# Performance work log

Measured on AMD Instinct MI355X. Metric: run time of the kernel, lower is better.

## Reference

```python
import jax, jax.numpy as jnp
import numpy as np

ALPHA_U = 1.0 / 10.0   # dt/tauu
ALPHA_V = 1.0 / 150.0  # dt/tauv
M = 10.0

def setup_inputs() -> dict:
    key = jax.random.key(0)
    ks = jax.random.split(key, 6)
    B, D_in, H = 8192, 1024, 2048
    stdv = 1.0 / np.sqrt(H)
    return {
        "x": jax.random.normal(ks[0], (B, D_in), dtype=jnp.float32),
        "u": jax.random.normal(ks[1], (B, H), dtype=jnp.float32),
        "v": jax.random.normal(ks[2], (B, H), dtype=jnp.float32),
        "win": jax.random.uniform(ks[3], (H, D_in), dtype=jnp.float32, minval=-stdv, maxval=stdv),
        "wr": jax.random.uniform(ks[4], (H, H), dtype=jnp.float32, minval=-stdv, maxval=stdv),
        "bias": jax.random.uniform(ks[5], (H,), dtype=jnp.float32, minval=-stdv, maxval=stdv),
    }

def reference(x, u, v, win, wr, bias):
    # v update: leaky blend toward m*u, then relu
    v_new = jax.nn.relu((1.0 - ALPHA_V) * v + (ALPHA_V * M) * u)
    # u update: leaky blend with input + recurrent drive minus adapted v
    drive = jnp.einsum('bi,hi->bh', x, win) + jnp.einsum('bk,hk->bh', u, wr) + bias - v_new
    u_new = jax.nn.relu((1.0 - ALPHA_U) * u + ALPHA_U * drive)
    return (u_new, v_new)
```

## Files before the change

### kernel.cpp

```cpp
#include <hip/hip_runtime.h>
#include <hip/hip_bf16.h>
#include <stdint.h>

#define B_DIM 8192
#define D_IN  1024
#define H_DIM 2048
#define K_DIM (D_IN + H_DIM)

#define CV_CONST  (1.0f - 1.0f/150.0f)
#define CUV_CONST (10.0f/150.0f)
#define CU_CONST  0.9f
#define AU_CONST  0.1f

typedef __attribute__((ext_vector_type(8))) short short8;
typedef __attribute__((ext_vector_type(4))) float floatx4;

__device__ __forceinline__ unsigned short f2bf(float f) {
    union { float f; unsigned u; } x; x.f = f;
    unsigned r = x.u + 0x7fffu + ((x.u >> 16) & 1u);
    return (unsigned short)(r >> 16);
}

#define N4_X   ((B_DIM * D_IN)  / 4)
#define N4_U   ((B_DIM * H_DIM) / 4)
#define N4_WIN ((H_DIM * D_IN)  / 4)
#define N4_WR  ((H_DIM * H_DIM) / 4)
#define N4_TOT (N4_X + N4_U + N4_WIN + N4_WR)

__global__ __launch_bounds__(256)
void pack_all(const float4* __restrict__ x, const float4* __restrict__ u,
              const float4* __restrict__ win, const float4* __restrict__ wr,
              unsigned short* __restrict__ Abf, unsigned short* __restrict__ Wbf) {
    int i = blockIdx.x * 256 + threadIdx.x;
    const float4* src; unsigned short* dst; int shift, mask, coloff;
    if (i < N4_X)                    { src = x;   dst = Abf; shift = 10; mask = 1023; coloff = 0;    }
    else if (i < N4_X + N4_U)        { i -= N4_X; src = u;   dst = Abf; shift = 11; mask = 2047; coloff = D_IN; }
    else if (i < N4_X + N4_U + N4_WIN){ i -= N4_X + N4_U; src = win; dst = Wbf; shift = 10; mask = 1023; coloff = 0; }
    else                             { i -= N4_X + N4_U + N4_WIN; src = wr; dst = Wbf; shift = 11; mask = 2047; coloff = D_IN; }
    int idx = i << 2;
    int r = idx >> shift;
    int c = idx & mask;
    float4 f = src[i];
    ushort4 o;
    o.x = f2bf(f.x); o.y = f2bf(f.y); o.z = f2bf(f.z); o.w = f2bf(f.w);
    *(ushort4*)(dst + (size_t)r * K_DIM + coloff + c) = o;
}

#define GLOAD_LDS16(gp, lp)                                                          \
    __builtin_amdgcn_global_load_lds(                                                \
        (const __attribute__((address_space(1))) unsigned int*)(gp),                 \
        (__attribute__((address_space(3))) unsigned int*)(lp), 16, 0, 0)

#define ES_STRIDE 68
#define ES_REGION (16 * ES_STRIDE)
#define SMEM_BYTES (8 * ES_REGION * 4)

__global__ __launch_bounds__(256, 4)
void gemm_fused(const unsigned short* __restrict__ A,
                const unsigned short* __restrict__ Wc,
                const float* __restrict__ u_in,
                const float* __restrict__ v_in,
                const float* __restrict__ bias,
                float* __restrict__ out)
{
    __shared__ __align__(16) unsigned char smem_raw[SMEM_BYTES];
    unsigned short* As = (unsigned short*)smem_raw;
    unsigned short* Bs = As + 128 * 32;
    float* Esf = (float*)smem_raw;

    const int tid  = threadIdx.x;
    const int wave = tid >> 6;
    const int lane = tid & 63;

    const int bid = blockIdx.x;
    const int wid = ((bid & 7) << 7) | (bid >> 3);
    const int bm = wid >> 4;
    const int bn = wid & 15;

    const int srow = lane >> 2;
    const int gcar = ((lane & 3) - ((lane >> 3) & 3)) & 3;
    const int scol = gcar * 8;
    const unsigned short* Ag = A  + (size_t)(bm * 128 + wave * 32 + srow) * K_DIM + scol;
    const unsigned short* Bg = Wc + (size_t)(bn * 128 + wave * 32 + srow) * K_DIM + scol;
    unsigned short* AsW = As + wave * 1024;
    unsigned short* BsW = Bs + wave * 1024;

    const int wm = (wave >> 1) * 64;
    const int wn = (wave & 1) * 64;
    const int frow = lane & 15;
    const int g    = lane >> 4;
    const int swz  = ((g + (frow >> 1)) & 3) * 8;

    floatx4 acc[4][4] = {};

    for (int k0 = 0; k0 < K_DIM; k0 += 32) {
        GLOAD_LDS16(Ag + k0,              AsW);
        GLOAD_LDS16(Ag + 16 * K_DIM + k0, AsW + 512);
        GLOAD_LDS16(Bg + k0,              BsW);
        GLOAD_LDS16(Bg + 16 * K_DIM + k0, BsW + 512);
        __syncthreads();

        short8 af[4], bfr[4];
#pragma unroll
        for (int i = 0; i < 4; i++)
            af[i] = *(const short8*)&As[(wm + i * 16 + frow) * 32 + swz];
#pragma unroll
        for (int j = 0; j < 4; j++)
            bfr[j] = *(const short8*)&Bs[(wn + j * 16 + frow) * 32 + swz];

#pragma unroll
        for (int i = 0; i < 4; i++)
#pragma unroll
            for (int j = 0; j < 4; j++)
                acc[i][j] = __builtin_amdgcn_mfma_f32_16x16x32_bf16(
                    af[i], bfr[j], acc[i][j], 0, 0, 0);
        __syncthreads();
    }

    const int q   = lane >> 4;
    const int c16 = lane & 15;
    const int rbase = q * 4;
    const int colg = bn * 128 + wn + c16 * 4;
    const float4 b4 = *(const float4*)&bias[colg];
    const size_t outV = (size_t)B_DIM * H_DIM;

#pragma unroll
    for (int i = 0; i < 4; i++) {
        float* Es = Esf + (wave * 2 + (i & 1)) * ES_REGION;
#pragma unroll
        for (int j = 0; j < 4; j++)
#pragma unroll
            for (int r = 0; r < 4; r++)
                Es[(rbase + r) * ES_STRIDE + j * 16 + c16] = acc[i][j][r];
#pragma unroll
        for (int rg = 0; rg < 4; rg++) {
            const int rloc = rg * 4 + q;
            const float4 a4 = *(const float4*)&Es[rloc * ES_STRIDE + c16 * 4];
            const size_t idx = (size_t)(bm * 128 + wm + i * 16 + rloc) * H_DIM + colg;
            const float4 u4 = *(const float4*)&u_in[idx];
            const float4 v4 = *(const float4*)&v_in[idx];
            float4 vn, un;
            vn.x = fmaxf(CV_CONST * v4.x + CUV_CONST * u4.x, 0.0f);
            vn.y = fmaxf(CV_CONST * v4.y + CUV_CONST * u4.y, 0.0f);
            vn.z = fmaxf(CV_CONST * v4.z + CUV_CONST * u4.z, 0.0f);
            vn.w = fmaxf(CV_CONST * v4.w + CUV_CONST * u4.w, 0.0f);
            un.x = fmaxf(CU_CONST * u4.x + AU_CONST * (a4.x + b4.x - vn.x), 0.0f);
            un.y = fmaxf(CU_CONST * u4.y + AU_CONST * (a4.y + b4.y - vn.y), 0.0f);
            un.z = fmaxf(CU_CONST * u4.z + AU_CONST * (a4.z + b4.z - vn.z), 0.0f);
            un.w = fmaxf(CU_CONST * u4.w + AU_CONST * (a4.w + b4.w - vn.w), 0.0f);
            *(float4*)&out[idx]        = un;
            *(float4*)&out[outV + idx] = vn;
        }
    }
}

extern "C" void kernel_launch(void* const* d_in, const int* in_sizes, int n_in,
                              void* d_out, int out_size, void* d_ws, size_t ws_size,
                              hipStream_t stream) {
    const float* x    = (const float*)d_in[0];
    const float* u    = (const float*)d_in[1];
    const float* v    = (const float*)d_in[2];
    const float* win  = (const float*)d_in[3];
    const float* wr   = (const float*)d_in[4];
    const float* bias = (const float*)d_in[5];
    float* out = (float*)d_out;

    unsigned short* Abf = (unsigned short*)d_ws;
    unsigned short* Wbf = Abf + (size_t)B_DIM * K_DIM;

    pack_all<<<N4_TOT / 256, 256, 0, stream>>>(
        (const float4*)x, (const float4*)u, (const float4*)win, (const float4*)wr,
        Abf, Wbf);

    gemm_fused<<<1024, 256, 0, stream>>>(Abf, Wbf, u, v, bias, out);
}
```

Baseline: 402.1 us.

## Rewrite GEMM as 256x256 tile, 8-wave double-buffered ping-pong pipeline

The fused GEMM kernel now uses 256x256 output tiles with 512 threads (8 waves) and 128 KB of LDS split into two K=64 stages. Each K step is divided into four quarter-phases, and each phase prefetches a slice of the next stage with global_load_lds. Explicit vmcnt/lgkmcnt waits, barriers and s_setprio bracket the MFMA bursts so loads overlap with matrix math. The goal is to raise arithmetic intensity and hide global latency, which the previous single-buffered 128x128, K=32 loop did poorly. The cost is heavy reliance on hand-tuned wait counts and a grid of only 256 blocks, so only one large block runs per CU.

After: 373.9 us. 1.08x faster.

```diff
diff --git a/kernel.cpp b/kernel.cpp
--- a/kernel.cpp
+++ b/kernel.cpp
@@ -51,11 +51,24 @@
         (const __attribute__((address_space(1))) unsigned int*)(gp),                 \
         (__attribute__((address_space(3))) unsigned int*)(lp), 16, 0, 0)
 
+#define VMCNT(n)  asm volatile("s_waitcnt vmcnt(" #n ")" ::: "memory")
+#define LGKM0     asm volatile("s_waitcnt lgkmcnt(0)" ::: "memory")
+#define SCHEDB    __builtin_amdgcn_sched_barrier(0)
+#define BAR       __builtin_amdgcn_s_barrier()
+#define PRIO1     __builtin_amdgcn_s_setprio(1)
+#define PRIO0     __builtin_amdgcn_s_setprio(0)
+
+#define NT (K_DIM / 64)
+
+#define ALO 0
+#define BLO 16384
+#define BHI 32768
+#define AHI 49152
+
 #define ES_STRIDE 68
 #define ES_REGION (16 * ES_STRIDE)
-#define SMEM_BYTES (8 * ES_REGION * 4)
-
-__global__ __launch_bounds__(256, 4)
+
+__global__ __launch_bounds__(512, 2)
 void gemm_fused(const unsigned short* __restrict__ A,
                 const unsigned short* __restrict__ Wc,
                 const float* __restrict__ u_in,
@@ -63,80 +76,206 @@
                 const float* __restrict__ bias,
                 float* __restrict__ out)
 {
-    __shared__ __align__(16) unsigned char smem_raw[SMEM_BYTES];
-    unsigned short* As = (unsigned short*)smem_raw;
-    unsigned short* Bs = As + 128 * 32;
-    float* Esf = (float*)smem_raw;
+    __shared__ __align__(16) unsigned char smem[131072];
 
     const int tid  = threadIdx.x;
     const int wave = tid >> 6;
     const int lane = tid & 63;
-
-    const int bid = blockIdx.x;
-    const int wid = ((bid & 7) << 7) | (bid >> 3);
-    const int bm = wid >> 4;
-    const int bn = wid & 15;
-
-    const int srow = lane >> 2;
-    const int gcar = ((lane & 3) - ((lane >> 3) & 3)) & 3;
-    const int scol = gcar * 8;
-    const unsigned short* Ag = A  + (size_t)(bm * 128 + wave * 32 + srow) * K_DIM + scol;
-    const unsigned short* Bg = Wc + (size_t)(bn * 128 + wave * 32 + srow) * K_DIM + scol;
-    unsigned short* AsW = As + wave * 1024;
-    unsigned short* BsW = Bs + wave * 1024;
-
-    const int wm = (wave >> 1) * 64;
-    const int wn = (wave & 1) * 64;
+    const int wrh  = wave >> 2;
+    const int wc   = wave & 3;
+
+    const int bid   = blockIdx.x;
+    const int wid   = ((bid & 7) << 5) | (bid >> 3);
+    const int tileM = (wid >> 3) << 8;
+    const int tileN = (wid & 7)  << 8;
+
     const int frow = lane & 15;
     const int g    = lane >> 4;
-    const int swz  = ((g + (frow >> 1)) & 3) * 8;
-
-    floatx4 acc[4][4] = {};
-
-    for (int k0 = 0; k0 < K_DIM; k0 += 32) {
-        GLOAD_LDS16(Ag + k0,              AsW);
-        GLOAD_LDS16(Ag + 16 * K_DIM + k0, AsW + 512);
-        GLOAD_LDS16(Bg + k0,              BsW);
-        GLOAD_LDS16(Bg + 16 * K_DIM + k0, BsW + 512);
-        __syncthreads();
-
-        short8 af[4], bfr[4];
-#pragma unroll
-        for (int i = 0; i < 4; i++)
-            af[i] = *(const short8*)&As[(wm + i * 16 + frow) * 32 + swz];
-#pragma unroll
-        for (int j = 0; j < 4; j++)
-            bfr[j] = *(const short8*)&Bs[(wn + j * 16 + frow) * 32 + swz];
-
-#pragma unroll
-        for (int i = 0; i < 4; i++)
-#pragma unroll
-            for (int j = 0; j < 4; j++)
-                acc[i][j] = __builtin_amdgcn_mfma_f32_16x16x32_bf16(
-                    af[i], bfr[j], acc[i][j], 0, 0, 0);
-        __syncthreads();
+
+    const unsigned short* Ag = A  + (size_t)(tileM + (wave >> 1) * 16 + frow) * K_DIM
+                                  + (wave & 1) * 32 + g * 8;
+    const unsigned short* Bg = Wc + (size_t)(tileN + (wave >> 2) * 64 + ((wave >> 1) & 1) * 16 + frow) * K_DIM
+                                  + (wave & 1) * 32 + g * 8;
+    const size_t R128 = (size_t)128 * K_DIM;
+    const size_t R64  = (size_t) 64 * K_DIM;
+    const size_t R32  = (size_t) 32 * K_DIM;
+
+    const int w1024 = wave << 10;
+
+    const int aRd = (wrh << 13) + (lane << 4);
+    const int bRd = (wc  << 12) + (lane << 4);
+
+    GLOAD_LDS16(Ag,               smem + ALO + w1024);
+    GLOAD_LDS16(Ag + R128,        smem + ALO + 8192 + w1024);
+    GLOAD_LDS16(Bg,               smem + BLO + w1024);
+    GLOAD_LDS16(Bg + R128,        smem + BLO + 8192 + w1024);
+    GLOAD_LDS16(Bg + R32,         smem + BHI + w1024);
+    GLOAD_LDS16(Bg + R32 + R128,  smem + BHI + 8192 + w1024);
+    GLOAD_LDS16(Ag + R64,         smem + AHI + w1024);
+    GLOAD_LDS16(Ag + R64 + R128,  smem + AHI + 8192 + w1024);
+
+    VMCNT(4);
+    BAR;
+    LGKM0;
+
+    floatx4 acc[8][4] = {};
+    short8 Ar[4][2], Bl[2][2], Bh[2][2];
+
+#define RD_A(cb, unit, i2s) (*(const short8*)(smem + (cb) + (unit) + aRd + (i2s) * 1024))
+#define RD_B(cb, unit, j2s) (*(const short8*)(smem + (cb) + (unit) + bRd + (j2s) * 1024))
+
+#pragma clang loop unroll(disable)
+    for (int t = 0; t < NT - 1; ++t) {
+        const int cb = (t & 1) << 16;
+        const int nb = cb ^ 65536;
+        const size_t kk = (size_t)(t + 1) * 64;
+
+        GLOAD_LDS16(Ag + kk,        smem + nb + ALO + w1024);
+        GLOAD_LDS16(Ag + kk + R128, smem + nb + ALO + 8192 + w1024);
+#pragma unroll
+        for (int i = 0; i < 4; ++i) { Ar[i][0] = RD_A(cb, ALO, i*2); Ar[i][1] = RD_A(cb, ALO, i*2+1); }
+#pragma unroll
+        for (int j = 0; j < 2; ++j) { Bl[j][0] = RD_B(cb, BLO, j*2); Bl[j][1] = RD_B(cb, BLO, j*2+1); }
+        VMCNT(4);
+        BAR; LGKM0; SCHEDB;
+        PRIO1;
+#pragma unroll
+        for (int i = 0; i < 4; ++i)
+#pragma unroll
+            for (int j = 0; j < 2; ++j) {
+                acc[i][j] = __builtin_amdgcn_mfma_f32_16x16x32_bf16(Ar[i][0], Bl[j][0], acc[i][j], 0, 0, 0);
+                acc[i][j] = __builtin_amdgcn_mfma_f32_16x16x32_bf16(Ar[i][1], Bl[j][1], acc[i][j], 0, 0, 0);
+            }
+        PRIO0; SCHEDB;
+        BAR;
+
+        GLOAD_LDS16(Bg + kk,        smem + nb + BLO + w1024);
+        GLOAD_LDS16(Bg + kk + R128, smem + nb + BLO + 8192 + w1024);
+#pragma unroll
+        for (int j = 0; j < 2; ++j) { Bh[j][0] = RD_B(cb, BHI, j*2); Bh[j][1] = RD_B(cb, BHI, j*2+1); }
+        VMCNT(4);
+        BAR; LGKM0; SCHEDB;
+        PRIO1;
+#pragma unroll
+        for (int i = 0; i < 4; ++i)
+#pragma unroll
+            for (int j = 0; j < 2; ++j) {
+                acc[i][2+j] = __builtin_amdgcn_mfma_f32_16x16x32_bf16(Ar[i][0], Bh[j][0], acc[i][2+j], 0, 0, 0);
+                acc[i][2+j] = __builtin_amdgcn_mfma_f32_16x16x32_bf16(Ar[i][1], Bh[j][1], acc[i][2+j], 0, 0, 0);
+            }
+        PRIO0; SCHEDB;
+        BAR;
+
+        GLOAD_LDS16(Bg + kk + R32,        smem + nb + BHI + w1024);
+        GLOAD_LDS16(Bg + kk + R32 + R128, smem + nb + BHI + 8192 + w1024);
+#pragma unroll
+        for (int i = 0; i < 4; ++i) { Ar[i][0] = RD_A(cb, AHI, i*2); Ar[i][1] = RD_A(cb, AHI, i*2+1); }
+        BAR; LGKM0; SCHEDB;
+        PRIO1;
+#pragma unroll
+        for (int i = 0; i < 4; ++i)
+#pragma unroll
+            for (int j = 0; j < 2; ++j) {
+                acc[4+i][2+j] = __builtin_amdgcn_mfma_f32_16x16x32_bf16(Ar[i][0], Bh[j][0], acc[4+i][2+j], 0, 0, 0);
+                acc[4+i][2+j] = __builtin_amdgcn_mfma_f32_16x16x32_bf16(Ar[i][1], Bh[j][1], acc[4+i][2+j], 0, 0, 0);
+            }
+        PRIO0; SCHEDB;
+        BAR;
+
+        GLOAD_LDS16(Ag + kk + R64,        smem + nb + AHI + w1024);
+        GLOAD_LDS16(Ag + kk + R64 + R128, smem + nb + AHI + 8192 + w1024);
+        VMCNT(4);
+        BAR; LGKM0; SCHEDB;
+        PRIO1;
+#pragma unroll
+        for (int i = 0; i < 4; ++i)
+#pragma unroll
+            for (int j = 0; j < 2; ++j) {
+                acc[4+i][j] = __builtin_amdgcn_mfma_f32_16x16x32_bf16(Ar[i][0], Bl[j][0], acc[4+i][j], 0, 0, 0);
+                acc[4+i][j] = __builtin_amdgcn_mfma_f32_16x16x32_bf16(Ar[i][1], Bl[j][1], acc[4+i][j], 0, 0, 0);
+            }
+        PRIO0; SCHEDB;
+        BAR;
     }
 
-    const int q   = lane >> 4;
-    const int c16 = lane & 15;
-    const int rbase = q * 4;
-    const int colg = bn * 128 + wn + c16 * 4;
+    {
+        const int cb = ((NT - 1) & 1) << 16;
+#pragma unroll
+        for (int i = 0; i < 4; ++i) { Ar[i][0] = RD_A(cb, ALO, i*2); Ar[i][1] = RD_A(cb, ALO, i*2+1); }
+#pragma unroll
+        for (int j = 0; j < 2; ++j) { Bl[j][0] = RD_B(cb, BLO, j*2); Bl[j][1] = RD_B(cb, BLO, j*2+1); }
+        VMCNT(2);
+        BAR; LGKM0; SCHEDB;
+        PRIO1;
+#pragma unroll
+        for (int i = 0; i < 4; ++i)
+#pragma unroll
+            for (int j = 0; j < 2; ++j) {
+                acc[i][j] = __builtin_amdgcn_mfma_f32_16x16x32_bf16(Ar[i][0], Bl[j][0], acc[i][j], 0, 0, 0);
+                acc[i][j] = __builtin_amdgcn_mfma_f32_16x16x32_bf16(Ar[i][1], Bl[j][1], acc[i][j], 0, 0, 0);
+            }
+        PRIO0; SCHEDB;
+        BAR;
+#pragma unroll
+        for (int j = 0; j < 2; ++j) { Bh[j][0] = RD_B(cb, BHI, j*2); Bh[j][1] = RD_B(cb, BHI, j*2+1); }
+        VMCNT(0);
+        BAR; LGKM0; SCHEDB;
+        PRIO1;
+#pragma unroll
+        for (int i = 0; i < 4; ++i)
+#pragma unroll
+            for (int j = 0; j < 2; ++j) {
+                acc[i][2+j] = __builtin_amdgcn_mfma_f32_16x16x32_bf16(Ar[i][0], Bh[j][0], acc[i][2+j], 0, 0, 0);
+                acc[i][2+j] = __builtin_amdgcn_mfma_f32_16x16x32_bf16(Ar[i][1], Bh[j][1], acc[i][2+j], 0, 0, 0);
+            }
+        PRIO0; SCHEDB;
+        BAR;
+#pragma unroll
+        for (int i = 0; i < 4; ++i) { Ar[i][0] = RD_A(cb, AHI, i*2); Ar[i][1] = RD_A(cb, AHI, i*2+1); }
+        BAR; LGKM0; SCHEDB;
+        PRIO1;
+#pragma unroll
+        for (int i = 0; i < 4; ++i)
+#pragma unroll
+            for (int j = 0; j < 2; ++j) {
+                acc[4+i][2+j] = __builtin_amdgcn_mfma_f32_16x16x32_bf16(Ar[i][0], Bh[j][0], acc[4+i][2+j], 0, 0, 0);
+                acc[4+i][2+j] = __builtin_amdgcn_mfma_f32_16x16x32_bf16(Ar[i][1], Bh[j][1], acc[4+i][2+j], 0, 0, 0);
+            }
+        PRIO0; SCHEDB;
+        BAR;
+        PRIO1;
+#pragma unroll
+        for (int i = 0; i < 4; ++i)
+#pragma unroll
+            for (int j = 0; j < 2; ++j) {
+                acc[4+i][j] = __builtin_amdgcn_mfma_f32_16x16x32_bf16(Ar[i][0], Bl[j][0], acc[4+i][j], 0, 0, 0);
+                acc[4+i][j] = __builtin_amdgcn_mfma_f32_16x16x32_bf16(Ar[i][1], Bl[j][1], acc[4+i][j], 0, 0, 0);
+            }
+        PRIO0;
+    }
+
+    __syncthreads();
+
+    float* Esf = (float*)smem;
+    const int q    = lane >> 4;
+    const int c16  = lane & 15;
+    const int colg = tileN + wc * 64 + c16 * 4;
     const float4 b4 = *(const float4*)&bias[colg];
     const size_t outV = (size_t)B_DIM * H_DIM;
 
 #pragma unroll
-    for (int i = 0; i < 4; i++) {
+    for (int i = 0; i < 8; ++i) {
         float* Es = Esf + (wave * 2 + (i & 1)) * ES_REGION;
 #pragma unroll
-        for (int j = 0; j < 4; j++)
-#pragma unroll
-            for (int r = 0; r < 4; r++)
-                Es[(rbase + r) * ES_STRIDE + j * 16 + c16] = acc[i][j][r];
+        for (int j = 0; j < 4; ++j)
+#pragma unroll
+            for (int r = 0; r < 4; ++r)
+                Es[(q * 4 + r) * ES_STRIDE + j * 16 + c16] = acc[i][j][r];
 #pragma unroll
         for (int rg = 0; rg < 4; rg++) {
             const int rloc = rg * 4 + q;
             const float4 a4 = *(const float4*)&Es[rloc * ES_STRIDE + c16 * 4];
-            const size_t idx = (size_t)(bm * 128 + wm + i * 16 + rloc) * H_DIM + colg;
+            const size_t idx = (size_t)(tileM + wrh * 128 + i * 16 + rloc) * H_DIM + colg;
             const float4 u4 = *(const float4*)&u_in[idx];
             const float4 v4 = *(const float4*)&v_in[idx];
             float4 vn, un;
@@ -172,5 +311,5 @@
         (const float4*)x, (const float4*)u, (const float4*)win, (const float4*)wr,
         Abf, Wbf);
 
-    gemm_fused<<<1024, 256, 0, stream>>>(Abf, Wbf, u, v, bias, out);
+    gemm_fused<<<256, 512, 0, stream>>>(Abf, Wbf, u, v, bias, out);
 }
```
